# Kernel tuning notes

Hardware: AMD Instinct MI355X
Metric: run time of the kernel (lower is better)

The kernel has to match this reference:

```python
import jax, jax.numpy as jnp
import numpy as np

L, H, NH, V, T, B, K = 12, 768, 12, 30522, 512, 4, 21
DH = H // NH
INV_SQRT_DH = 1.0 / float(np.sqrt(DH))
NEG = -1e4  # BERT additive mask value
LN_EPS = 1e-12


def _ln(x, g, b):
    m = x.mean(-1, keepdims=True)
    v = jnp.var(x, axis=-1, keepdims=True)
    return (x - m) * jax.lax.rsqrt(v + LN_EPS) * g + b


def _encoder(input_ids, attention_mask, word_emb, pos_emb, tok_emb, emb_g, emb_b,
             Wqkv, bqkv, Wo, bo, ln1_g, ln1_b, W1, b1, W2, b2, ln2_g, ln2_b):
    Bv, Tv = input_ids.shape
    h = word_emb[input_ids] + pos_emb[None, :Tv] + tok_emb[0]  # token_type_ids = 0
    h = _ln(h, emb_g, emb_b)
    bias = (1.0 - attention_mask[:, None, None, :].astype(h.dtype)) * NEG  # [B,1,1,T]

    def layer(h, xs):
        wqkv, bq, wo, bo_, g1, b1_, w1, bb1, w2, bb2, g2, b2_ = xs
        qkv = h @ wqkv + bq  # [B,T,3H]
        q, k, v = jnp.split(qkv, 3, axis=-1)
        def hd(x):
            return x.reshape(Bv, Tv, NH, DH).transpose(0, 2, 1, 3)
        q, k, v = hd(q), hd(k), hd(v)
        scores = jnp.einsum('bhqd,bhkd->bhqk', q, k) * INV_SQRT_DH + bias
        ctx = jnp.einsum('bhqk,bhkd->bhqd', jax.nn.softmax(scores, axis=-1), v)
        ctx = ctx.transpose(0, 2, 1, 3).reshape(Bv, Tv, H)
        h = _ln(h + ctx @ wo + bo_, g1, b1_)  # post-LN (BERT)
        ff = jax.nn.gelu(h @ w1 + bb1, approximate=False) @ w2 + bb2
        h = _ln(h + ff, g2, b2_)
        return h, None

    h, _ = jax.lax.scan(layer, h, (Wqkv, bqkv, Wo, bo, ln1_g, ln1_b, W1, b1, W2, b2, ln2_g, ln2_b))
    return h


def _crf_nll(emissions, tags, mask, start, end, trans):
    # emissions [B,T,K], tags [B,T] int, mask [B,T] bool; torchcrf reduction='mean'
    Bv, Tv, Kv = emissions.shape
    maskf = mask.astype(emissions.dtype)
    # numerator: score of the gold path
    num = start[tags[:, 0]] + emissions[jnp.arange(Bv), 0, tags[:, 0]]
    em_t = jnp.take_along_axis(emissions, tags[..., None], axis=-1)[..., 0]  # [B,T]
    tr_t = trans[tags[:, :-1], tags[:, 1:]]  # [B,T-1]
    num = num + jnp.sum((tr_t + em_t[:, 1:]) * maskf[:, 1:], axis=1)
    last_idx = mask.sum(axis=1).astype(jnp.int32) - 1
    last_tag = jnp.take_along_axis(tags, last_idx[:, None], axis=1)[:, 0]
    num = num + end[last_tag]
    # denominator: forward algorithm (logsumexp recursion over time)
    alpha0 = start[None, :] + emissions[:, 0]  # [B,K]

    def step(alpha, xs):
        em, m = xs  # em [B,K], m [B] bool
        nxt = jax.scipy.special.logsumexp(alpha[:, :, None] + trans[None] + em[:, None, :], axis=1)
        return jnp.where(m[:, None], nxt, alpha), None

    alpha, _ = jax.lax.scan(step, alpha0, (emissions[:, 1:].transpose(1, 0, 2), mask[:, 1:].T))
    den = jax.scipy.special.logsumexp(alpha + end[None, :], axis=1)
    return -(num - den).mean()


def _viterbi(emissions, mask, start, end, trans):
    # Returns [B,T] int32 best paths; padded tail repeats the last valid tag.
    Bv, Tv, Kv = emissions.shape
    score0 = start[None, :] + emissions[:, 0]
    ident = jnp.broadcast_to(jnp.arange(Kv), (Bv, Kv))

    def step(score, xs):
        em, m = xs
        cand = score[:, :, None] + trans[None]  # [B,K_prev,K_next]
        idx = jnp.where(m[:, None], jnp.argmax(cand, axis=1), ident)
        nxt = jnp.max(cand, axis=1) + em
        return jnp.where(m[:, None], nxt, score), idx

    score, hist = jax.lax.scan(step, score0, (emissions[:, 1:].transpose(1, 0, 2), mask[:, 1:].T))
    last = jnp.argmax(score + end[None, :], axis=1)  # [B]

    def back(nxt_tag, idx):
        prev = jnp.take_along_axis(idx, nxt_tag[:, None], axis=1)[:, 0]
        return prev, nxt_tag

    tag0, rest = jax.lax.scan(back, last, hist, reverse=True)  # rest[i] = tag at t=i+1
    return jnp.concatenate([tag0[None], rest], axis=0).T.astype(jnp.int32)


def setup_inputs():
    key = jax.random.key(0)
    ks = jax.random.split(key, 16)
    s = 0.02

    def n(k, shape):
        return (s * jax.random.normal(k, shape)).astype(jnp.float32)

    def u(k, shape):
        return jax.random.uniform(k, shape, minval=-0.1, maxval=0.1).astype(jnp.float32)

    p = {}
    p['input_ids'] = jax.random.randint(ks[0], (B, T), 0, V)
    lengths = jax.random.randint(ks[1], (B,), T // 2, T + 1)
    p['attention_mask'] = (jnp.arange(T)[None, :] < lengths[:, None]).astype(jnp.int32)
    p['valid_mask'] = p['attention_mask']
    p['labels'] = jax.random.randint(ks[2], (B, T), 0, K)
    p['word_emb'] = n(ks[3], (V, H))
    p['pos_emb'] = n(ks[4], (T, H))
    p['tok_emb'] = n(ks[5], (2, H))
    p['emb_g'] = jnp.ones((H,), jnp.float32)
    p['emb_b'] = jnp.zeros((H,), jnp.float32)
    p['Wqkv'] = n(ks[6], (L, H, 3 * H))
    p['bqkv'] = jnp.zeros((L, 3 * H), jnp.float32)
    p['Wo'] = n(ks[7], (L, H, H))
    p['bo'] = jnp.zeros((L, H), jnp.float32)
    p['ln1_g'] = jnp.ones((L, H), jnp.float32)
    p['ln1_b'] = jnp.zeros((L, H), jnp.float32)
    p['W1'] = n(ks[8], (L, H, 4 * H))
    p['b1'] = jnp.zeros((L, 4 * H), jnp.float32)
    p['W2'] = n(ks[9], (L, 4 * H, H))
    p['b2'] = jnp.zeros((L, H), jnp.float32)
    p['ln2_g'] = jnp.ones((L, H), jnp.float32)
    p['ln2_b'] = jnp.zeros((L, H), jnp.float32)
    p['Wc'] = n(ks[10], (H, K))
    p['bc'] = jnp.zeros((K,), jnp.float32)
    p['crf_start'] = u(ks[11], (K,))
    p['crf_end'] = u(ks[12], (K,))
    p['crf_trans'] = u(ks[13], (K, K))
    return p


def reference(input_ids, attention_mask, valid_mask, labels,
              word_emb, pos_emb, tok_emb, emb_g, emb_b,
              Wqkv, bqkv, Wo, bo, ln1_g, ln1_b, W1, b1, W2, b2, ln2_g, ln2_b,
              Wc, bc, crf_start, crf_end, crf_trans):
    h = _encoder(input_ids, attention_mask, word_emb, pos_emb, tok_emb, emb_g, emb_b,
                 Wqkv, bqkv, Wo, bo, ln1_g, ln1_b, W1, b1, W2, b2, ln2_g, ln2_b)
    emissions = h @ Wc + bc  # dropout is identity in eval/reference mode
    mask = attention_mask.astype(bool)
    nll = _crf_nll(emissions, labels, mask, crf_start, crf_end, crf_trans)
    decoded = _viterbi(emissions, mask, crf_start, crf_end, crf_trans)
    return nll, decoded
```

## Files before the change

kernel.cpp:

```cpp
#include <hip/hip_runtime.h>
#include <math.h>

constexpr int NLAYER = 12;
constexpr int H = 768;
constexpr int NH = 12;
constexpr int DH = 64;
constexpr int T = 512;
constexpr int B = 4;
constexpr int K = 21;
constexpr int BT = B * T;
constexpr float NEGB = -10000.0f;
constexpr float LNEPS = 1e-12f;
constexpr float INV_SQRT_DH = 0.125f;

typedef __attribute__((ext_vector_type(8))) short bf16x8;
typedef __attribute__((ext_vector_type(4))) float f32x4;
typedef __attribute__((ext_vector_type(4))) unsigned short u16x4;

#define WAIT_VMCNT(n) asm volatile("s_waitcnt vmcnt(" #n ")")

__device__ __forceinline__ float wave_sum_f(float v) {
#pragma unroll
  for (int off = 32; off > 0; off >>= 1) v += __shfl_xor(v, off);
  return v;
}
__device__ __forceinline__ int wave_sum_i(int v) {
#pragma unroll
  for (int off = 32; off > 0; off >>= 1) v += __shfl_xor(v, off);
  return v;
}
__device__ __forceinline__ float readlane_f(float v, int i) {
  return __uint_as_float(__builtin_amdgcn_readlane(__float_as_uint(v), i));
}
__device__ __forceinline__ unsigned short f32_bf16_rn(float x) {
  unsigned int u = __float_as_uint(x);
  u += 0x7fffu + ((u >> 16) & 1u);
  return (unsigned short)(u >> 16);
}
__device__ __forceinline__ void split_bf16(float x, unsigned short& h, unsigned short& l) {
  h = f32_bf16_rn(x);
  float hf = __uint_as_float((unsigned int)h << 16);
  l = f32_bf16_rn(x - hf);
}
__device__ __forceinline__ void block_reduce_sum2(float& s, float& q) {
  __shared__ float red[8];
  s = wave_sum_f(s);
  q = wave_sum_f(q);
  int lane = threadIdx.x & 63, wid = threadIdx.x >> 6;
  if (lane == 0) { red[wid] = s; red[4 + wid] = q; }
  __syncthreads();
  s = red[0] + red[1] + red[2] + red[3];
  q = red[4] + red[5] + red[6] + red[7];
}

__global__ __launch_bounds__(256) void embed_ln_kernel(
    const int* __restrict__ ids, const float* __restrict__ wemb,
    const float* __restrict__ pemb, const float* __restrict__ temb,
    const float* __restrict__ g, const float* __restrict__ bta,
    float* __restrict__ h, unsigned short* __restrict__ hh,
    unsigned short* __restrict__ hl) {
  int row = blockIdx.x;
  int t = row % T;
  int id = ids[row];
  const float* wp = wemb + (size_t)id * H;
  const float* pp = pemb + (size_t)t * H;
  float x[3];
  float s = 0.f, q = 0.f;
#pragma unroll
  for (int i = 0; i < 3; i++) {
    int c = threadIdx.x + i * 256;
    x[i] = wp[c] + pp[c] + temb[c];
    s += x[i];
    q += x[i] * x[i];
  }
  block_reduce_sum2(s, q);
  float mean = s * (1.0f / H);
  float var = q * (1.0f / H) - mean * mean;
  float inv = rsqrtf(var + LNEPS);
#pragma unroll
  for (int i = 0; i < 3; i++) {
    int c = threadIdx.x + i * 256;
    float y = (x[i] - mean) * inv * g[c] + bta[c];
    h[(size_t)row * H + c] = y;
    unsigned short yh, yl;
    split_bf16(y, yh, yl);
    hh[(size_t)row * H + c] = yh;
    hl[(size_t)row * H + c] = yl;
  }
}

__global__ __launch_bounds__(256) void add_ln_kernel(
    float* __restrict__ h, const float* __restrict__ add,
    const float* __restrict__ g, const float* __restrict__ bta,
    unsigned short* __restrict__ hh, unsigned short* __restrict__ hl) {
  int row = blockIdx.x;
  size_t base = (size_t)row * H;
  float x[3];
  float s = 0.f, q = 0.f;
#pragma unroll
  for (int i = 0; i < 3; i++) {
    int c = threadIdx.x + i * 256;
    x[i] = h[base + c] + add[base + c];
    s += x[i];
    q += x[i] * x[i];
  }
  block_reduce_sum2(s, q);
  float mean = s * (1.0f / H);
  float var = q * (1.0f / H) - mean * mean;
  float inv = rsqrtf(var + LNEPS);
#pragma unroll
  for (int i = 0; i < 3; i++) {
    int c = threadIdx.x + i * 256;
    float y = (x[i] - mean) * inv * g[c] + bta[c];
    h[base + c] = y;
    unsigned short yh, yl;
    split_bf16(y, yh, yl);
    hh[base + c] = yh;
    hl[base + c] = yl;
  }
}

__global__ __launch_bounds__(256) void wconv_kernel(
    const float* __restrict__ w0, const float* __restrict__ w1,
    const float* __restrict__ w2, const float* __restrict__ w3,
    unsigned short* __restrict__ Wth, unsigned short* __restrict__ Wtl) {
  __shared__ float tile[32][33];
  int bid = blockIdx.x;
  const float* src;
  int Kd, N, tk, tn;
  size_t off;
  if (bid < 1728) {
    src = w0; Kd = 768; N = 2304; tk = bid / 72; tn = bid % 72; off = 0;
  } else if (bid < 2304) {
    int t2 = bid - 1728; src = w1; Kd = 768; N = 768; tk = t2 / 24; tn = t2 % 24;
    off = 1769472;
  } else if (bid < 4608) {
    int t2 = bid - 2304; src = w2; Kd = 768; N = 3072; tk = t2 / 96; tn = t2 % 96;
    off = 2359296;
  } else {
    int t2 = bid - 4608; src = w3; Kd = 3072; N = 768; tk = t2 / 24; tn = t2 % 24;
    off = 4718592;
  }
  int tid = threadIdx.x;
  int k0 = tk * 32, n0 = tn * 32;
  int r = tid >> 3, c = (tid & 7) * 4;
  float4 v = *(const float4*)(src + (size_t)(k0 + r) * N + n0 + c);
  tile[r][c + 0] = v.x; tile[r][c + 1] = v.y; tile[r][c + 2] = v.z; tile[r][c + 3] = v.w;
  __syncthreads();
  u16x4 hv, lv;
#pragma unroll
  for (int q2 = 0; q2 < 4; q2++) {
    unsigned short sh, sl;
    split_bf16(tile[c + q2][r], sh, sl);
    hv[q2] = sh; lv[q2] = sl;
  }
  size_t dst = off + (size_t)(n0 + r) * Kd + k0 + c;
  *(u16x4*)(Wth + dst) = hv;
  *(u16x4*)(Wtl + dst) = lv;
}

template <int BN, bool GELU, bool SPLITOUT>
__global__ __launch_bounds__(256) void gemm_bf3_kernel(
    const unsigned short* __restrict__ Ah, const unsigned short* __restrict__ Al,
    const unsigned short* __restrict__ Wth, const unsigned short* __restrict__ Wtl,
    const float* __restrict__ bias, float* __restrict__ C,
    unsigned short* __restrict__ Ch, unsigned short* __restrict__ Cl,
    int N, int Kd) {
  constexpr int WN = BN / 2;
  constexpr int FN = WN / 16;
  constexpr int AW = 128 * 32;
  constexpr int WW = BN * 32;
  constexpr int DBS = 2 * AW + 2 * WW;
  __shared__ short lds_s[2 * DBS];
  int tid = threadIdx.x;
  int lane = tid & 63, wid = tid >> 6;
  int wr = wid >> 1, wc = wid & 1;
  int bm = blockIdx.y * 128, bn = blockIdx.x * BN;
  f32x4 acc[4][FN] = {};
  int lrow = lane >> 2;
  int lslot_sw = (lane & 3) ^ ((lrow >> 1) & 3);

  const unsigned short* sbase;
  int rowbase, ldsoff, nchunks;
  if (wid == 0)      { sbase = Ah;  rowbase = bm; ldsoff = 0;            nchunks = 8; }
  else if (wid == 1) { sbase = Al;  rowbase = bm; ldsoff = AW;           nchunks = 8; }
  else if (wid == 2) { sbase = Wth; rowbase = bn; ldsoff = 2 * AW;       nchunks = BN / 16; }
  else               { sbase = Wtl; rowbase = bn; ldsoff = 2 * AW + WW;  nchunks = BN / 16; }

  const unsigned short* srcbase = sbase + (size_t)(rowbase + lrow) * Kd + lslot_sw * 8;

  auto STAGE = [&](int db, int k0) {
#pragma unroll
    for (int c = 0; c < 8; c++) {
      if (c < nchunks) {
        const unsigned short* src = srcbase + (size_t)(c * 16) * Kd + k0;
        char* dst = ((char*)lds_s) + (db * DBS + ldsoff) * 2 + c * 1024 + lane * 16;
        __builtin_amdgcn_global_load_lds(
            (const __attribute__((address_space(1))) void*)src,
            (__attribute__((address_space(3))) void*)dst, 16, 0, 0);
      }
    }
  };

  const int NT = Kd / 32;
  STAGE(0, 0);
  for (int kt = 0; kt < NT; kt++) {
    int cur = kt & 1;
    bool more = (kt + 1 < NT);
    if (more) STAGE(cur ^ 1, (kt + 1) * 32);
    if (more) {
      if (BN == 128 || wid < 2) { WAIT_VMCNT(8); } else { WAIT_VMCNT(4); }
    } else {
      WAIT_VMCNT(0);
    }
    __builtin_amdgcn_s_barrier();
    __builtin_amdgcn_sched_barrier(0);

    int lr = lane & 15, lg = lane >> 4;
    int slot = (lg ^ ((lr >> 1) & 3)) * 8;
    int cb = cur * DBS;
    bf16x8 af_h[4], af_l[4], wf_h[FN], wf_l[FN];
#pragma unroll
    for (int i = 0; i < 4; i++) {
      int e = (wr * 64 + i * 16 + lr) * 32 + slot;
      af_h[i] = *(const bf16x8*)&lds_s[cb + e];
      af_l[i] = *(const bf16x8*)&lds_s[cb + AW + e];
    }
#pragma unroll
    for (int j = 0; j < FN; j++) {
      int e = (wc * WN + j * 16 + lr) * 32 + slot;
      wf_h[j] = *(const bf16x8*)&lds_s[cb + 2 * AW + e];
      wf_l[j] = *(const bf16x8*)&lds_s[cb + 2 * AW + WW + e];
    }
#pragma unroll
    for (int i = 0; i < 4; i++)
#pragma unroll
      for (int j = 0; j < FN; j++) {
        acc[i][j] = __builtin_amdgcn_mfma_f32_16x16x32_bf16(af_h[i], wf_h[j], acc[i][j], 0, 0, 0);
        acc[i][j] = __builtin_amdgcn_mfma_f32_16x16x32_bf16(af_l[i], wf_h[j], acc[i][j], 0, 0, 0);
        acc[i][j] = __builtin_amdgcn_mfma_f32_16x16x32_bf16(af_h[i], wf_l[j], acc[i][j], 0, 0, 0);
      }
    asm volatile("s_waitcnt lgkmcnt(0)");
    __builtin_amdgcn_sched_barrier(0);
    __builtin_amdgcn_s_barrier();
    __builtin_amdgcn_sched_barrier(0);
  }

  int lr = lane & 15, lg = lane >> 4;
#pragma unroll
  for (int i = 0; i < 4; i++) {
#pragma unroll
    for (int j = 0; j < FN; j++) {
      int row = bm + wr * 64 + i * 16 + lg * 4;
      int col = bn + wc * WN + j * 16 + lr;
      float bv = bias[col];
#pragma unroll
      for (int r = 0; r < 4; r++) {
        float v = acc[i][j][r] + bv;
        if (GELU) v = 0.5f * v * (1.0f + erff(v * 0.70710678118654752f));
        if (SPLITOUT) {
          unsigned short sh, sl;
          split_bf16(v, sh, sl);
          Ch[(size_t)(row + r) * N + col] = sh;
          Cl[(size_t)(row + r) * N + col] = sl;
        } else {
          C[(size_t)(row + r) * N + col] = v;
        }
      }
    }
  }
}

__global__ __launch_bounds__(256) void qk_kernel(
    const float* __restrict__ qkv, const int* __restrict__ mask,
    float* __restrict__ S) {
  int bh = blockIdx.z;
  int b = bh / NH, hh = bh % NH;
  int i0 = blockIdx.y * 64, j0 = blockIdx.x * 64;
  __shared__ float Qs[64][64];
  __shared__ float Ks[64][64];
  int tid = threadIdx.x;
  int r = tid >> 2;
  int cseg = (tid & 3) * 16;
  const float* qbase = qkv + (size_t)(b * T + i0 + r) * (3 * H) + hh * DH;
  const float* kbase = qkv + (size_t)(b * T + j0 + r) * (3 * H) + H + hh * DH;
#pragma unroll
  for (int ss = 0; ss < 4; ss++) {
    int c = cseg + ss * 4;
    float4 qa = *(const float4*)(qbase + c);
    float4 ka = *(const float4*)(kbase + c);
    Qs[c + 0][r] = qa.x; Qs[c + 1][r] = qa.y; Qs[c + 2][r] = qa.z; Qs[c + 3][r] = qa.w;
    Ks[c + 0][r] = ka.x; Ks[c + 1][r] = ka.y; Ks[c + 2][r] = ka.z; Ks[c + 3][r] = ka.w;
  }
  __syncthreads();
  int tx = tid & 15, ty = tid >> 4;
  float acc[4][4] = {};
#pragma unroll 4
  for (int d = 0; d < 64; d++) {
    float a_[4], b_[4];
    *(float4*)a_ = *(const float4*)&Qs[d][ty * 4];
    *(float4*)b_ = *(const float4*)&Ks[d][tx * 4];
#pragma unroll
    for (int i = 0; i < 4; i++)
#pragma unroll
      for (int j = 0; j < 4; j++)
        acc[i][j] = fmaf(a_[i], b_[j], acc[i][j]);
  }
  float bj[4];
#pragma unroll
  for (int q = 0; q < 4; q++)
    bj[q] = (1.0f - (float)mask[b * T + j0 + tx * 4 + q]) * NEGB;
#pragma unroll
  for (int i = 0; i < 4; i++) {
    int gi = i0 + ty * 4 + i;
    int gj = j0 + tx * 4;
    float4 o;
    o.x = acc[i][0] * INV_SQRT_DH + bj[0];
    o.y = acc[i][1] * INV_SQRT_DH + bj[1];
    o.z = acc[i][2] * INV_SQRT_DH + bj[2];
    o.w = acc[i][3] * INV_SQRT_DH + bj[3];
    *(float4*)(S + ((size_t)bh * T + gi) * T + gj) = o;
  }
}

__global__ __launch_bounds__(128) void softmax_kernel(float* __restrict__ S) {
  size_t row = blockIdx.x;
  float* p = S + row * T;
  int tid = threadIdx.x;
  float4 v = *(float4*)(p + tid * 4);
  float m = fmaxf(fmaxf(v.x, v.y), fmaxf(v.z, v.w));
#pragma unroll
  for (int off = 32; off > 0; off >>= 1) m = fmaxf(m, __shfl_xor(m, off));
  __shared__ float redm[2];
  __shared__ float reds[2];
  int wid = tid >> 6;
  if ((tid & 63) == 0) redm[wid] = m;
  __syncthreads();
  m = fmaxf(redm[0], redm[1]);
  v.x = __expf(v.x - m);
  v.y = __expf(v.y - m);
  v.z = __expf(v.z - m);
  v.w = __expf(v.w - m);
  float s = v.x + v.y + v.z + v.w;
  s = wave_sum_f(s);
  if ((tid & 63) == 0) reds[wid] = s;
  __syncthreads();
  s = reds[0] + reds[1];
  float inv = 1.0f / s;
  v.x *= inv; v.y *= inv; v.z *= inv; v.w *= inv;
  *(float4*)(p + tid * 4) = v;
}

__global__ __launch_bounds__(256) void pv_kernel(
    const float* __restrict__ S, const float* __restrict__ qkv,
    unsigned short* __restrict__ cth, unsigned short* __restrict__ ctl) {
  int bh = blockIdx.y;
  int b = bh / NH, hh = bh % NH;
  int i0 = blockIdx.x * 64;
  __shared__ float Ps[64][68];
  __shared__ float Vs[64][64];
  int tid = threadIdx.x;
  int r = tid >> 2;
  int cseg = (tid & 3) * 16;
  int tx = tid & 15, ty = tid >> 4;
  float acc[4][4] = {};
  const float* srow = S + ((size_t)bh * T + i0 + r) * T;
  const float* vbase = qkv + (size_t)(b * T) * (3 * H) + 2 * H + hh * DH;
  for (int k0 = 0; k0 < T; k0 += 64) {
    __syncthreads();
#pragma unroll
    for (int ss = 0; ss < 4; ss++) {
      int c = cseg + ss * 4;
      *(float4*)&Ps[r][c] = *(const float4*)(srow + k0 + c);
      *(float4*)&Vs[r][c] = *(const float4*)(vbase + (size_t)(k0 + r) * (3 * H) + c);
    }
    __syncthreads();
#pragma unroll
    for (int kk = 0; kk < 64; kk += 4) {
      float p_[4][4], v_[4][4];
#pragma unroll
      for (int i = 0; i < 4; i++)
        *(float4*)p_[i] = *(const float4*)&Ps[ty * 4 + i][kk];
#pragma unroll
      for (int s = 0; s < 4; s++)
        *(float4*)v_[s] = *(const float4*)&Vs[kk + s][tx * 4];
#pragma unroll
      for (int i = 0; i < 4; i++)
#pragma unroll
        for (int s = 0; s < 4; s++)
#pragma unroll
          for (int j = 0; j < 4; j++)
            acc[i][j] = fmaf(p_[i][s], v_[s][j], acc[i][j]);
    }
  }
#pragma unroll
  for (int i = 0; i < 4; i++) {
    int gi = i0 + ty * 4 + i;
    size_t idx = (size_t)(b * T + gi) * H + hh * DH + tx * 4;
    u16x4 hv, lv;
#pragma unroll
    for (int j = 0; j < 4; j++) {
      unsigned short sh, sl;
      split_bf16(acc[i][j], sh, sl);
      hv[j] = sh; lv[j] = sl;
    }
    *(u16x4*)(cth + idx) = hv;
    *(u16x4*)(ctl + idx) = lv;
  }
}

__global__ __launch_bounds__(256) void classifier_kernel(
    const float* __restrict__ h, const float* __restrict__ Wc,
    const float* __restrict__ bc, float* __restrict__ em) {
  int id = blockIdx.x * 256 + threadIdx.x;
  if (id >= BT * K) return;
  int row = id / K, k = id % K;
  float acc = bc[k];
  const float* hr = h + (size_t)row * H;
  for (int d = 0; d < H; d++) acc = fmaf(hr[d], Wc[d * K + k], acc);
  em[id] = acc;
}

#define MRG(vo, io, va, ia, vb, ib) \
  float vo = ((vb) > (va)) ? (vb) : (va); \
  int io = ((vb) > (va)) ? (ib) : (ia);

__global__ __launch_bounds__(64) void crf_fused_kernel(
    const float* __restrict__ em, const int* __restrict__ labels,
    const int* __restrict__ mask, const float* __restrict__ start,
    const float* __restrict__ endv, const float* __restrict__ trans,
    float* __restrict__ parts, float* __restrict__ outdec) {
  __shared__ float em_s[T * K];
  __shared__ int mask_s[T];
  __shared__ unsigned char hist_s[(T - 1) * K];
  __shared__ float sc_s[32];
  int b = blockIdx.x & 3;
  int role = blockIdx.x >> 2;
  int j = threadIdx.x;
  const float* eb = em + (size_t)b * T * K;
  for (int i = j; i < T * K / 4; i += 64)
    ((float4*)em_s)[i] = ((const float4*)eb)[i];
  for (int i = j; i < T; i += 64) mask_s[i] = mask[b * T + i];
  __syncthreads();
  bool act = (j < K);
  float tr[K];
#pragma unroll
  for (int i = 0; i < K; i++) tr[i] = act ? trans[i * K + j] : 0.f;

  int cntloc = 0;
  for (int t = j; t < T; t += 64) cntloc += mask_s[t];
  int cnt = wave_sum_i(cntloc);

  if (role == 0) {
    const int* tb = labels + b * T;
    float numloc = 0.f;
    for (int t = j; t < T; t += 64) {
      if (t >= 1 && mask_s[t]) {
        int tp = tb[t - 1], tc = tb[t];
        numloc += trans[tp * K + tc] + em_s[t * K + tc];
      }
    }
    float num = wave_sum_f(numloc);
    float etr[K];
#pragma unroll
    for (int i = 0; i < K; i++) etr[i] = __expf(tr[i]);
    float alpha = act ? (start[j] + em_s[j]) : 0.f;
    float emv = act ? em_s[K + j] : 0.f;
    for (int t = 1; t < cnt; t++) {
      float emv_n = (act && (t + 1) < cnt) ? em_s[(t + 1) * K + j] : 0.f;
      float m0 = readlane_f(alpha, 0);
      float ee = __expf(alpha - m0);
      float e0 = readlane_f(ee, 0),  e1 = readlane_f(ee, 1),  e2 = readlane_f(ee, 2);
      float e3 = readlane_f(ee, 3),  e4 = readlane_f(ee, 4),  e5 = readlane_f(ee, 5);
      float e6 = readlane_f(ee, 6),  e7 = readlane_f(ee, 7),  e8 = readlane_f(ee, 8);
      float e9 = readlane_f(ee, 9),  e10 = readlane_f(ee, 10), e11 = readlane_f(ee, 11);
      float e12 = readlane_f(ee, 12), e13 = readlane_f(ee, 13), e14 = readlane_f(ee, 14);
      float e15 = readlane_f(ee, 15), e16 = readlane_f(ee, 16), e17 = readlane_f(ee, 17);
      float e18 = readlane_f(ee, 18), e19 = readlane_f(ee, 19), e20 = readlane_f(ee, 20);
      float a0 = fmaf(e16, etr[16], fmaf(e12, etr[12], fmaf(e8, etr[8],  fmaf(e4, etr[4], e0 * etr[0]))));
      float a1 = fmaf(e17, etr[17], fmaf(e13, etr[13], fmaf(e9, etr[9],  fmaf(e5, etr[5], e1 * etr[1]))));
      float a2 = fmaf(e18, etr[18], fmaf(e14, etr[14], fmaf(e10, etr[10], fmaf(e6, etr[6], e2 * etr[2]))));
      float a3 = fmaf(e19, etr[19], fmaf(e15, etr[15], fmaf(e11, etr[11], fmaf(e7, etr[7], e3 * etr[3]))));
      float ssum = fmaf(e20, etr[20], (a0 + a1) + (a2 + a3));
      float nxt = __logf(ssum) + m0 + emv;
      if (act) alpha = nxt;
      emv = emv_n;
    }
    float aj = act ? (alpha + endv[j]) : -3.0e38f;
    float mm = aj;
#pragma unroll
    for (int off = 32; off > 0; off >>= 1) mm = fmaxf(mm, __shfl_xor(mm, off));
    float e2v = act ? __expf(aj - mm) : 0.f;
    float s2 = wave_sum_f(e2v);
    float den = __logf(s2) + mm;
    if (j == 0) {
      int tag0 = tb[0];
      float numtot = num + start[tag0] + em_s[tag0] + endv[tb[cnt - 1]];
      parts[b] = numtot - den;
    }
  } else {
    float score = act ? (start[j] + em_s[j]) : 0.f;
    float emv = act ? em_s[K + j] : 0.f;
    for (int t = 1; t < cnt; t++) {
      float emv_n = (act && (t + 1) < cnt) ? em_s[(t + 1) * K + j] : 0.f;
      float c0 = readlane_f(score, 0) + tr[0],   c1 = readlane_f(score, 1) + tr[1];
      float c2 = readlane_f(score, 2) + tr[2],   c3 = readlane_f(score, 3) + tr[3];
      float c4 = readlane_f(score, 4) + tr[4],   c5 = readlane_f(score, 5) + tr[5];
      float c6 = readlane_f(score, 6) + tr[6],   c7 = readlane_f(score, 7) + tr[7];
      float c8 = readlane_f(score, 8) + tr[8],   c9 = readlane_f(score, 9) + tr[9];
      float c10 = readlane_f(score, 10) + tr[10], c11 = readlane_f(score, 11) + tr[11];
      float c12 = readlane_f(score, 12) + tr[12], c13 = readlane_f(score, 13) + tr[13];
      float c14 = readlane_f(score, 14) + tr[14], c15 = readlane_f(score, 15) + tr[15];
      float c16 = readlane_f(score, 16) + tr[16], c17 = readlane_f(score, 17) + tr[17];
      float c18 = readlane_f(score, 18) + tr[18], c19 = readlane_f(score, 19) + tr[19];
      float c20 = readlane_f(score, 20) + tr[20];
      MRG(m0v, m0i, c0, 0, c1, 1)
      MRG(m1v, m1i, c2, 2, c3, 3)
      MRG(m2v, m2i, c4, 4, c5, 5)
      MRG(m3v, m3i, c6, 6, c7, 7)
      MRG(m4v, m4i, c8, 8, c9, 9)
      MRG(m5v, m5i, c10, 10, c11, 11)
      MRG(m6v, m6i, c12, 12, c13, 13)
      MRG(m7v, m7i, c14, 14, c15, 15)
      MRG(m8v, m8i, c16, 16, c17, 17)
      MRG(m9v, m9i, c18, 18, c19, 19)
      MRG(p0v, p0i, m0v, m0i, m1v, m1i)
      MRG(p1v, p1i, m2v, m2i, m3v, m3i)
      MRG(p2v, p2i, m4v, m4i, m5v, m5i)
      MRG(p3v, p3i, m6v, m6i, m7v, m7i)
      MRG(p4v, p4i, m8v, m8i, m9v, m9i)
      MRG(r0v, r0i, p0v, p0i, p1v, p1i)
      MRG(r1v, r1i, p2v, p2i, p3v, p3i)
      MRG(r2v, r2i, p4v, p4i, c20, 20)
      MRG(s0v, s0i, r0v, r0i, r1v, r1i)
      MRG(fv, fi, s0v, s0i, r2v, r2i)
      if (act) {
        hist_s[(t - 1) * K + j] = (unsigned char)fi;
        score = fv + emv;
      }
      emv = emv_n;
    }
    if (act) sc_s[j] = score + endv[j];
    __syncthreads();
    if (j == 0) {
      float best = -3.0e38f;
      int last = 0;
#pragma unroll
      for (int i = 0; i < K; i++)
        if (sc_s[i] > best) { best = sc_s[i]; last = i; }
      for (int t = cnt - 1; t < T; t++) outdec[b * T + t] = (float)last;
      int cur = last;
      for (int t = cnt - 1; t >= 1; t--) {
        cur = hist_s[(t - 1) * K + cur];
        outdec[b * T + (t - 1)] = (float)cur;
      }
    }
  }
}

__global__ void nll_final_kernel(const float* __restrict__ parts,
                                 float* __restrict__ out) {
  out[0] = -0.25f * (parts[0] + parts[1] + parts[2] + parts[3]);
}

extern "C" void kernel_launch(void* const* d_in, const int* in_sizes, int n_in,
                              void* d_out, int out_size, void* d_ws, size_t ws_size,
                              hipStream_t stream) {
  (void)in_sizes; (void)n_in; (void)out_size; (void)ws_size;
  const int* ids    = (const int*)d_in[0];
  const int* amask  = (const int*)d_in[1];
  const int* labels = (const int*)d_in[3];
  const float* wemb = (const float*)d_in[4];
  const float* pemb = (const float*)d_in[5];
  const float* temb = (const float*)d_in[6];
  const float* eg   = (const float*)d_in[7];
  const float* ebta = (const float*)d_in[8];
  const float* Wqkv = (const float*)d_in[9];
  const float* bqkv = (const float*)d_in[10];
  const float* Wo   = (const float*)d_in[11];
  const float* bo   = (const float*)d_in[12];
  const float* ln1g = (const float*)d_in[13];
  const float* ln1b = (const float*)d_in[14];
  const float* W1   = (const float*)d_in[15];
  const float* b1   = (const float*)d_in[16];
  const float* W2   = (const float*)d_in[17];
  const float* b2   = (const float*)d_in[18];
  const float* ln2g = (const float*)d_in[19];
  const float* ln2b = (const float*)d_in[20];
  const float* Wc   = (const float*)d_in[21];
  const float* bc   = (const float*)d_in[22];
  const float* cst  = (const float*)d_in[23];
  const float* cen  = (const float*)d_in[24];
  const float* ctr  = (const float*)d_in[25];
  float* out = (float*)d_out;

  float* ws = (float*)d_ws;
  float* h    = ws;
  unsigned short* hh = (unsigned short*)(h + 1572864);
  unsigned short* hl = (unsigned short*)(h + 1572864 + 786432);
  float* qkv  = h + 1572864 + 786432 * 2;
  unsigned short* cth = (unsigned short*)(qkv + 4718592);
  unsigned short* ctl = (unsigned short*)(qkv + 4718592 + 786432);
  float* tmp  = qkv + 4718592 + 786432 * 2;
  float* big  = tmp + 1572864;
  unsigned short* gh = (unsigned short*)(big + 12582912);
  unsigned short* gl = (unsigned short*)(big + 12582912 + 3145728);
  unsigned short* Wth = (unsigned short*)(big + 12582912 + 3145728 * 2);
  unsigned short* Wtl = (unsigned short*)(big + 12582912 + 3145728 * 2 + 3538944);
  float* em   = big + 12582912 + 3145728 * 2 + 3538944 * 2;
  float* parts = em + 43008;

  embed_ln_kernel<<<BT, 256, 0, stream>>>(ids, wemb, pemb, temb, eg, ebta, h, hh, hl);

  for (int l = 0; l < NLAYER; l++) {
    const float* bqkv_l = bqkv + (size_t)l * 3 * H;
    const float* bo_l   = bo + (size_t)l * H;
    const float* b1_l   = b1 + (size_t)l * 4 * H;
    const float* b2_l   = b2 + (size_t)l * H;

    wconv_kernel<<<6912, 256, 0, stream>>>(
        Wqkv + (size_t)l * H * 3 * H, Wo + (size_t)l * H * H,
        W1 + (size_t)l * H * 4 * H, W2 + (size_t)l * 4 * H * H, Wth, Wtl);

    gemm_bf3_kernel<128, false, false><<<dim3(18, 16), 256, 0, stream>>>(
        hh, hl, Wth, Wtl, bqkv_l, qkv, nullptr, nullptr, 3 * H, H);
    qk_kernel<<<dim3(T / 64, T / 64, B * NH), 256, 0, stream>>>(qkv, amask, big);
    softmax_kernel<<<B * NH * T, 128, 0, stream>>>(big);
    pv_kernel<<<dim3(T / 64, B * NH), 256, 0, stream>>>(big, qkv, cth, ctl);
    gemm_bf3_kernel<64, false, false><<<dim3(12, 16), 256, 0, stream>>>(
        cth, ctl, Wth + 1769472, Wtl + 1769472, bo_l, tmp, nullptr, nullptr, H, H);
    add_ln_kernel<<<BT, 256, 0, stream>>>(h, tmp, ln1g + (size_t)l * H, ln1b + (size_t)l * H, hh, hl);
    gemm_bf3_kernel<128, true, true><<<dim3(24, 16), 256, 0, stream>>>(
        hh, hl, Wth + 2359296, Wtl + 2359296, b1_l, nullptr, gh, gl, 4 * H, H);
    gemm_bf3_kernel<64, false, false><<<dim3(12, 16), 256, 0, stream>>>(
        gh, gl, Wth + 4718592, Wtl + 4718592, b2_l, tmp, nullptr, nullptr, H, 4 * H);
    add_ln_kernel<<<BT, 256, 0, stream>>>(h, tmp, ln2g + (size_t)l * H, ln2b + (size_t)l * H, hh, hl);
  }

  classifier_kernel<<<(BT * K + 255) / 256, 256, 0, stream>>>(h, Wc, bc, em);
  crf_fused_kernel<<<8, 64, 0, stream>>>(em, labels, amask, cst, cen, ctr, parts, out + 1);
  nll_final_kernel<<<1, 1, 0, stream>>>(parts, out);
}
```

Baseline: 3.251 ms.

## Fuse attention into flash-style MFMA kernel with head-major split-bf16 QKV epilogue

Replaces the separate fp32 QK^T, softmax and PV kernels with a single flash-attention kernel. It uses online softmax and bf16x3 MFMA for both the score and PV products, and keeps probabilities in LDS. The QKV GEMM epilogue now writes Q/K head-major and V transposed as hi/lo bf16 splits, which removes the large B*NH*T*T score buffer traffic and the fp32 SIMT FMA loops. The cost is uncoalesced scalar stores in the QKV epilogue and per-tile global K/V reloads without LDS staging.

```diff
diff --git a/kernel.cpp b/kernel.cpp
--- a/kernel.cpp
+++ b/kernel.cpp
@@ -159,12 +159,14 @@
   *(u16x4*)(Wtl + dst) = lv;
 }
 
-template <int BN, bool GELU, bool SPLITOUT>
+template <int BN, int OUTMODE>
 __global__ __launch_bounds__(256) void gemm_bf3_kernel(
     const unsigned short* __restrict__ Ah, const unsigned short* __restrict__ Al,
     const unsigned short* __restrict__ Wth, const unsigned short* __restrict__ Wtl,
     const float* __restrict__ bias, float* __restrict__ C,
     unsigned short* __restrict__ Ch, unsigned short* __restrict__ Cl,
+    unsigned short* __restrict__ Kh, unsigned short* __restrict__ Kl,
+    unsigned short* __restrict__ Vth, unsigned short* __restrict__ Vtl,
     int N, int Kd) {
   constexpr int WN = BN / 2;
   constexpr int FN = WN / 16;
@@ -254,158 +256,181 @@
       int row = bm + wr * 64 + i * 16 + lg * 4;
       int col = bn + wc * WN + j * 16 + lr;
       float bv = bias[col];
-#pragma unroll
-      for (int r = 0; r < 4; r++) {
-        float v = acc[i][j][r] + bv;
-        if (GELU) v = 0.5f * v * (1.0f + erff(v * 0.70710678118654752f));
-        if (SPLITOUT) {
-          unsigned short sh, sl;
-          split_bf16(v, sh, sl);
-          Ch[(size_t)(row + r) * N + col] = sh;
-          Cl[(size_t)(row + r) * N + col] = sl;
+      if (OUTMODE == 2) {
+        int sec = col / 768;
+        int within = col % 768;
+        int hidx = within >> 6, d = within & 63;
+        int b = row >> 9, t = row & 511;
+        int bh = b * NH + hidx;
+        if (sec == 2) {
+          u16x4 hv, lv;
+#pragma unroll
+          for (int r = 0; r < 4; r++) {
+            unsigned short sh, sl;
+            split_bf16(acc[i][j][r] + bv, sh, sl);
+            hv[r] = sh; lv[r] = sl;
+          }
+          size_t idx = ((size_t)bh * 64 + d) * T + t;
+          *(u16x4*)(Vth + idx) = hv;
+          *(u16x4*)(Vtl + idx) = lv;
         } else {
-          C[(size_t)(row + r) * N + col] = v;
+          unsigned short* dh = (sec == 0) ? Ch : Kh;
+          unsigned short* dl = (sec == 0) ? Cl : Kl;
+#pragma unroll
+          for (int r = 0; r < 4; r++) {
+            unsigned short sh, sl;
+            split_bf16(acc[i][j][r] + bv, sh, sl);
+            size_t idx = ((size_t)bh * T + t + r) * 64 + d;
+            dh[idx] = sh;
+            dl[idx] = sl;
+          }
         }
-      }
-    }
-  }
-}
-
-__global__ __launch_bounds__(256) void qk_kernel(
-    const float* __restrict__ qkv, const int* __restrict__ mask,
-    float* __restrict__ S) {
-  int bh = blockIdx.z;
-  int b = bh / NH, hh = bh % NH;
-  int i0 = blockIdx.y * 64, j0 = blockIdx.x * 64;
-  __shared__ float Qs[64][64];
-  __shared__ float Ks[64][64];
-  int tid = threadIdx.x;
-  int r = tid >> 2;
-  int cseg = (tid & 3) * 16;
-  const float* qbase = qkv + (size_t)(b * T + i0 + r) * (3 * H) + hh * DH;
-  const float* kbase = qkv + (size_t)(b * T + j0 + r) * (3 * H) + H + hh * DH;
-#pragma unroll
-  for (int ss = 0; ss < 4; ss++) {
-    int c = cseg + ss * 4;
-    float4 qa = *(const float4*)(qbase + c);
-    float4 ka = *(const float4*)(kbase + c);
-    Qs[c + 0][r] = qa.x; Qs[c + 1][r] = qa.y; Qs[c + 2][r] = qa.z; Qs[c + 3][r] = qa.w;
-    Ks[c + 0][r] = ka.x; Ks[c + 1][r] = ka.y; Ks[c + 2][r] = ka.z; Ks[c + 3][r] = ka.w;
-  }
-  __syncthreads();
-  int tx = tid & 15, ty = tid >> 4;
-  float acc[4][4] = {};
-#pragma unroll 4
-  for (int d = 0; d < 64; d++) {
-    float a_[4], b_[4];
-    *(float4*)a_ = *(const float4*)&Qs[d][ty * 4];
-    *(float4*)b_ = *(const float4*)&Ks[d][tx * 4];
-#pragma unroll
-    for (int i = 0; i < 4; i++)
-#pragma unroll
-      for (int j = 0; j < 4; j++)
-        acc[i][j] = fmaf(a_[i], b_[j], acc[i][j]);
-  }
-  float bj[4];
-#pragma unroll
-  for (int q = 0; q < 4; q++)
-    bj[q] = (1.0f - (float)mask[b * T + j0 + tx * 4 + q]) * NEGB;
-#pragma unroll
-  for (int i = 0; i < 4; i++) {
-    int gi = i0 + ty * 4 + i;
-    int gj = j0 + tx * 4;
-    float4 o;
-    o.x = acc[i][0] * INV_SQRT_DH + bj[0];
-    o.y = acc[i][1] * INV_SQRT_DH + bj[1];
-    o.z = acc[i][2] * INV_SQRT_DH + bj[2];
-    o.w = acc[i][3] * INV_SQRT_DH + bj[3];
-    *(float4*)(S + ((size_t)bh * T + gi) * T + gj) = o;
-  }
-}
-
-__global__ __launch_bounds__(128) void softmax_kernel(float* __restrict__ S) {
-  size_t row = blockIdx.x;
-  float* p = S + row * T;
-  int tid = threadIdx.x;
-  float4 v = *(float4*)(p + tid * 4);
-  float m = fmaxf(fmaxf(v.x, v.y), fmaxf(v.z, v.w));
-#pragma unroll
-  for (int off = 32; off > 0; off >>= 1) m = fmaxf(m, __shfl_xor(m, off));
-  __shared__ float redm[2];
-  __shared__ float reds[2];
-  int wid = tid >> 6;
-  if ((tid & 63) == 0) redm[wid] = m;
-  __syncthreads();
-  m = fmaxf(redm[0], redm[1]);
-  v.x = __expf(v.x - m);
-  v.y = __expf(v.y - m);
-  v.z = __expf(v.z - m);
-  v.w = __expf(v.w - m);
-  float s = v.x + v.y + v.z + v.w;
-  s = wave_sum_f(s);
-  if ((tid & 63) == 0) reds[wid] = s;
-  __syncthreads();
-  s = reds[0] + reds[1];
-  float inv = 1.0f / s;
-  v.x *= inv; v.y *= inv; v.z *= inv; v.w *= inv;
-  *(float4*)(p + tid * 4) = v;
-}
-
-__global__ __launch_bounds__(256) void pv_kernel(
-    const float* __restrict__ S, const float* __restrict__ qkv,
+      } else {
+#pragma unroll
+        for (int r = 0; r < 4; r++) {
+          float v = acc[i][j][r] + bv;
+          if (OUTMODE == 1) {
+            v = 0.5f * v * (1.0f + erff(v * 0.70710678118654752f));
+            unsigned short sh, sl;
+            split_bf16(v, sh, sl);
+            Ch[(size_t)(row + r) * N + col] = sh;
+            Cl[(size_t)(row + r) * N + col] = sl;
+          } else {
+            C[(size_t)(row + r) * N + col] = v;
+          }
+        }
+      }
+    }
+  }
+}
+
+__global__ __launch_bounds__(256) void attn_kernel(
+    const unsigned short* __restrict__ qh, const unsigned short* __restrict__ ql,
+    const unsigned short* __restrict__ kh, const unsigned short* __restrict__ kl,
+    const unsigned short* __restrict__ vth, const unsigned short* __restrict__ vtl,
+    const int* __restrict__ mask,
     unsigned short* __restrict__ cth, unsigned short* __restrict__ ctl) {
   int bh = blockIdx.y;
-  int b = bh / NH, hh = bh % NH;
+  int b = bh / NH, hidx = bh % NH;
   int i0 = blockIdx.x * 64;
-  __shared__ float Ps[64][68];
-  __shared__ float Vs[64][64];
-  int tid = threadIdx.x;
-  int r = tid >> 2;
-  int cseg = (tid & 3) * 16;
-  int tx = tid & 15, ty = tid >> 4;
-  float acc[4][4] = {};
-  const float* srow = S + ((size_t)bh * T + i0 + r) * T;
-  const float* vbase = qkv + (size_t)(b * T) * (3 * H) + 2 * H + hh * DH;
-  for (int k0 = 0; k0 < T; k0 += 64) {
-    __syncthreads();
-#pragma unroll
-    for (int ss = 0; ss < 4; ss++) {
-      int c = cseg + ss * 4;
-      *(float4*)&Ps[r][c] = *(const float4*)(srow + k0 + c);
-      *(float4*)&Vs[r][c] = *(const float4*)(vbase + (size_t)(k0 + r) * (3 * H) + c);
-    }
-    __syncthreads();
-#pragma unroll
-    for (int kk = 0; kk < 64; kk += 4) {
-      float p_[4][4], v_[4][4];
-#pragma unroll
-      for (int i = 0; i < 4; i++)
-        *(float4*)p_[i] = *(const float4*)&Ps[ty * 4 + i][kk];
-#pragma unroll
-      for (int s = 0; s < 4; s++)
-        *(float4*)v_[s] = *(const float4*)&Vs[kk + s][tx * 4];
-#pragma unroll
-      for (int i = 0; i < 4; i++)
-#pragma unroll
-        for (int s = 0; s < 4; s++)
-#pragma unroll
-          for (int j = 0; j < 4; j++)
-            acc[i][j] = fmaf(p_[i][s], v_[s][j], acc[i][j]);
-    }
-  }
-#pragma unroll
-  for (int i = 0; i < 4; i++) {
-    int gi = i0 + ty * 4 + i;
-    size_t idx = (size_t)(b * T + gi) * H + hh * DH + tx * 4;
-    u16x4 hv, lv;
-#pragma unroll
-    for (int j = 0; j < 4; j++) {
+  int tid = threadIdx.x, lane = tid & 63, w = tid >> 6;
+  int lr = lane & 15, lg = lane >> 4;
+  __shared__ float bias_s[T];
+  __shared__ short p_h[4][16 * 64];
+  __shared__ short p_l[4][16 * 64];
+  for (int i = tid; i < T; i += 256)
+    bias_s[i] = (1.0f - (float)mask[b * T + i]) * NEGB;
+  __syncthreads();
+
+  const unsigned short* qb_h = qh + ((size_t)bh * T + i0 + w * 16 + lr) * 64 + lg * 8;
+  const unsigned short* qb_l = ql + ((size_t)bh * T + i0 + w * 16 + lr) * 64 + lg * 8;
+  bf16x8 qf_h0 = *(const bf16x8*)qb_h;
+  bf16x8 qf_h1 = *(const bf16x8*)(qb_h + 32);
+  bf16x8 qf_l0 = *(const bf16x8*)qb_l;
+  bf16x8 qf_l1 = *(const bf16x8*)(qb_l + 32);
+
+  float m_run[4], l_run[4];
+#pragma unroll
+  for (int r = 0; r < 4; r++) { m_run[r] = -3.0e38f; l_run[r] = 0.f; }
+  f32x4 acc_o[4] = {};
+
+  for (int kt = 0; kt < T / 64; kt++) {
+    f32x4 s[4] = {};
+#pragma unroll
+    for (int jf = 0; jf < 4; jf++) {
+      size_t kb = ((size_t)bh * T + kt * 64 + jf * 16 + lr) * 64 + lg * 8;
+      bf16x8 kf_h0 = *(const bf16x8*)(kh + kb);
+      bf16x8 kf_h1 = *(const bf16x8*)(kh + kb + 32);
+      bf16x8 kf_l0 = *(const bf16x8*)(kl + kb);
+      bf16x8 kf_l1 = *(const bf16x8*)(kl + kb + 32);
+      s[jf] = __builtin_amdgcn_mfma_f32_16x16x32_bf16(qf_h0, kf_h0, s[jf], 0, 0, 0);
+      s[jf] = __builtin_amdgcn_mfma_f32_16x16x32_bf16(qf_h1, kf_h1, s[jf], 0, 0, 0);
+      s[jf] = __builtin_amdgcn_mfma_f32_16x16x32_bf16(qf_l0, kf_h0, s[jf], 0, 0, 0);
+      s[jf] = __builtin_amdgcn_mfma_f32_16x16x32_bf16(qf_l1, kf_h1, s[jf], 0, 0, 0);
+      s[jf] = __builtin_amdgcn_mfma_f32_16x16x32_bf16(qf_h0, kf_l0, s[jf], 0, 0, 0);
+      s[jf] = __builtin_amdgcn_mfma_f32_16x16x32_bf16(qf_h1, kf_l1, s[jf], 0, 0, 0);
+    }
+    float mt[4] = {-3.0e38f, -3.0e38f, -3.0e38f, -3.0e38f};
+#pragma unroll
+    for (int jf = 0; jf < 4; jf++) {
+      float bcol = bias_s[kt * 64 + jf * 16 + lr];
+#pragma unroll
+      for (int r = 0; r < 4; r++) {
+        float v = s[jf][r] * INV_SQRT_DH + bcol;
+        s[jf][r] = v;
+        mt[r] = fmaxf(mt[r], v);
+      }
+    }
+#pragma unroll
+    for (int r = 0; r < 4; r++) {
+      mt[r] = fmaxf(mt[r], __shfl_xor(mt[r], 1));
+      mt[r] = fmaxf(mt[r], __shfl_xor(mt[r], 2));
+      mt[r] = fmaxf(mt[r], __shfl_xor(mt[r], 4));
+      mt[r] = fmaxf(mt[r], __shfl_xor(mt[r], 8));
+    }
+#pragma unroll
+    for (int r = 0; r < 4; r++) {
+      float mn = fmaxf(m_run[r], mt[r]);
+      float sc = __expf(m_run[r] - mn);
+      m_run[r] = mn;
+      l_run[r] *= sc;
+#pragma unroll
+      for (int jf = 0; jf < 4; jf++) acc_o[jf][r] *= sc;
+    }
+    float ps[4] = {0.f, 0.f, 0.f, 0.f};
+#pragma unroll
+    for (int jf = 0; jf < 4; jf++) {
+#pragma unroll
+      for (int r = 0; r < 4; r++) {
+        float p = __expf(s[jf][r] - m_run[r]);
+        ps[r] += p;
+        unsigned short sh, sl;
+        split_bf16(p, sh, sl);
+        int q = lg * 4 + r;
+        int col = jf * 16 + lr;
+        int addr = q * 64 + (((col >> 3) ^ (q & 7)) << 3) + (col & 7);
+        p_h[w][addr] = sh;
+        p_l[w][addr] = sl;
+      }
+    }
+#pragma unroll
+    for (int r = 0; r < 4; r++) {
+      ps[r] += __shfl_xor(ps[r], 1);
+      ps[r] += __shfl_xor(ps[r], 2);
+      ps[r] += __shfl_xor(ps[r], 4);
+      ps[r] += __shfl_xor(ps[r], 8);
+      l_run[r] += ps[r];
+    }
+#pragma unroll
+    for (int c = 0; c < 2; c++) {
+      int aaddr = lr * 64 + (((4 * c + lg) ^ (lr & 7)) << 3);
+      bf16x8 pa_h = *(const bf16x8*)&p_h[w][aaddr];
+      bf16x8 pa_l = *(const bf16x8*)&p_l[w][aaddr];
+#pragma unroll
+      for (int jf = 0; jf < 4; jf++) {
+        size_t vb = ((size_t)bh * 64 + jf * 16 + lr) * T + kt * 64 + c * 32 + lg * 8;
+        bf16x8 vf_h = *(const bf16x8*)(vth + vb);
+        bf16x8 vf_l = *(const bf16x8*)(vtl + vb);
+        acc_o[jf] = __builtin_amdgcn_mfma_f32_16x16x32_bf16(pa_h, vf_h, acc_o[jf], 0, 0, 0);
+        acc_o[jf] = __builtin_amdgcn_mfma_f32_16x16x32_bf16(pa_l, vf_h, acc_o[jf], 0, 0, 0);
+        acc_o[jf] = __builtin_amdgcn_mfma_f32_16x16x32_bf16(pa_h, vf_l, acc_o[jf], 0, 0, 0);
+      }
+    }
+  }
+  float inv[4];
+#pragma unroll
+  for (int r = 0; r < 4; r++) inv[r] = 1.0f / l_run[r];
+#pragma unroll
+  for (int jf = 0; jf < 4; jf++) {
+#pragma unroll
+    for (int r = 0; r < 4; r++) {
+      float v = acc_o[jf][r] * inv[r];
       unsigned short sh, sl;
-      split_bf16(acc[i][j], sh, sl);
-      hv[j] = sh; lv[j] = sl;
-    }
-    *(u16x4*)(cth + idx) = hv;
-    *(u16x4*)(ctl + idx) = lv;
+      split_bf16(v, sh, sl);
+      size_t idx = ((size_t)(b * T) + i0 + w * 16 + lg * 4 + r) * H + hidx * 64 + jf * 16 + lr;
+      cth[idx] = sh;
+      ctl[idx] = sl;
+    }
   }
 }
 
@@ -595,20 +620,25 @@
   float* out = (float*)d_out;
 
   float* ws = (float*)d_ws;
-  float* h    = ws;
-  unsigned short* hh = (unsigned short*)(h + 1572864);
-  unsigned short* hl = (unsigned short*)(h + 1572864 + 786432);
-  float* qkv  = h + 1572864 + 786432 * 2;
-  unsigned short* cth = (unsigned short*)(qkv + 4718592);
-  unsigned short* ctl = (unsigned short*)(qkv + 4718592 + 786432);
-  float* tmp  = qkv + 4718592 + 786432 * 2;
-  float* big  = tmp + 1572864;
-  unsigned short* gh = (unsigned short*)(big + 12582912);
-  unsigned short* gl = (unsigned short*)(big + 12582912 + 3145728);
-  unsigned short* Wth = (unsigned short*)(big + 12582912 + 3145728 * 2);
-  unsigned short* Wtl = (unsigned short*)(big + 12582912 + 3145728 * 2 + 3538944);
-  float* em   = big + 12582912 + 3145728 * 2 + 3538944 * 2;
-  float* parts = em + 43008;
+  float* fp = ws;
+  float* h = fp;                 fp += 1572864;
+  unsigned short* hh  = (unsigned short*)fp; fp += 786432;
+  unsigned short* hl  = (unsigned short*)fp; fp += 786432;
+  unsigned short* qhp = (unsigned short*)fp; fp += 786432;
+  unsigned short* qlp = (unsigned short*)fp; fp += 786432;
+  unsigned short* khp = (unsigned short*)fp; fp += 786432;
+  unsigned short* klp = (unsigned short*)fp; fp += 786432;
+  unsigned short* vtp = (unsigned short*)fp; fp += 786432;
+  unsigned short* vlp = (unsigned short*)fp; fp += 786432;
+  unsigned short* cth = (unsigned short*)fp; fp += 786432;
+  unsigned short* ctl = (unsigned short*)fp; fp += 786432;
+  float* tmp = fp;               fp += 1572864;
+  unsigned short* gh  = (unsigned short*)fp; fp += 3145728;
+  unsigned short* gl  = (unsigned short*)fp; fp += 3145728;
+  unsigned short* Wth = (unsigned short*)fp; fp += 3538944;
+  unsigned short* Wtl = (unsigned short*)fp; fp += 3538944;
+  float* em = fp;                fp += 43008;
+  float* parts = fp;
 
   embed_ln_kernel<<<BT, 256, 0, stream>>>(ids, wemb, pemb, temb, eg, ebta, h, hh, hl);
 
@@ -622,18 +652,20 @@
         Wqkv + (size_t)l * H * 3 * H, Wo + (size_t)l * H * H,
         W1 + (size_t)l * H * 4 * H, W2 + (size_t)l * 4 * H * H, Wth, Wtl);
 
-    gemm_bf3_kernel<128, false, false><<<dim3(18, 16), 256, 0, stream>>>(
-        hh, hl, Wth, Wtl, bqkv_l, qkv, nullptr, nullptr, 3 * H, H);
-    qk_kernel<<<dim3(T / 64, T / 64, B * NH), 256, 0, stream>>>(qkv, amask, big);
-    softmax_kernel<<<B * NH * T, 128, 0, stream>>>(big);
-    pv_kernel<<<dim3(T / 64, B * NH), 256, 0, stream>>>(big, qkv, cth, ctl);
-    gemm_bf3_kernel<64, false, false><<<dim3(12, 16), 256, 0, stream>>>(
-        cth, ctl, Wth + 1769472, Wtl + 1769472, bo_l, tmp, nullptr, nullptr, H, H);
+    gemm_bf3_kernel<128, 2><<<dim3(18, 16), 256, 0, stream>>>(
+        hh, hl, Wth, Wtl, bqkv_l, nullptr, qhp, qlp, khp, klp, vtp, vlp, 3 * H, H);
+    attn_kernel<<<dim3(T / 64, B * NH), 256, 0, stream>>>(
+        qhp, qlp, khp, klp, vtp, vlp, amask, cth, ctl);
+    gemm_bf3_kernel<64, 0><<<dim3(12, 16), 256, 0, stream>>>(
+        cth, ctl, Wth + 1769472, Wtl + 1769472, bo_l, tmp,
+        nullptr, nullptr, nullptr, nullptr, nullptr, nullptr, H, H);
     add_ln_kernel<<<BT, 256, 0, stream>>>(h, tmp, ln1g + (size_t)l * H, ln1b + (size_t)l * H, hh, hl);
-    gemm_bf3_kernel<128, true, true><<<dim3(24, 16), 256, 0, stream>>>(
-        hh, hl, Wth + 2359296, Wtl + 2359296, b1_l, nullptr, gh, gl, 4 * H, H);
-    gemm_bf3_kernel<64, false, false><<<dim3(12, 16), 256, 0, stream>>>(
-        gh, gl, Wth + 4718592, Wtl + 4718592, b2_l, tmp, nullptr, nullptr, H, 4 * H);
+    gemm_bf3_kernel<128, 1><<<dim3(24, 16), 256, 0, stream>>>(
+        hh, hl, Wth + 2359296, Wtl + 2359296, b1_l, nullptr, gh, gl,
+        nullptr, nullptr, nullptr, nullptr, 4 * H, H);
+    gemm_bf3_kernel<64, 0><<<dim3(12, 16), 256, 0, stream>>>(
+        gh, gl, Wth + 4718592, Wtl + 4718592, b2_l, tmp,
+        nullptr, nullptr, nullptr, nullptr, nullptr, nullptr, H, 4 * H);
     add_ln_kernel<<<BT, 256, 0, stream>>>(h, tmp, ln2g + (size_t)l * H, ln2b + (size_t)l * H, hh, hl);
   }
 
```

Result: no change. 3.278 ms (+0.8%).
